# Performance work log

Measured on AMD Instinct MI355X. Metric: run time of the kernel, lower is better.

Reference implementation:

```python
import jax, jax.numpy as jnp
import numpy as np

B, T, C = 2, 4096, 512
H, DH = 8, 64            # num_heads, num_head_channels (per-head dim after reshape)
COND = 512
SCALE = (DH // H) ** -0.5  # faithful to original: (num_head_channels // num_heads)**-0.5


def setup_inputs() -> dict:
    key = jax.random.key(0)
    ks = jax.random.split(key, 6)
    x = jax.random.normal(ks[0], (B, T, C), dtype=jnp.float32)
    condition = jax.random.normal(ks[1], (B, T, COND), dtype=jnp.float32)
    W_qk = jax.random.normal(ks[2], (COND, 2 * H * DH), dtype=jnp.float32) * (COND ** -0.5)
    W_v = jax.random.normal(ks[3], (C, H * DH), dtype=jnp.float32) * (C ** -0.5)
    W_u = jax.random.normal(ks[4], (H * DH, C), dtype=jnp.float32) * ((H * DH) ** -0.5)
    b_u = jax.random.normal(ks[5], (C,), dtype=jnp.float32) * 0.01
    return {"x": x, "condition": condition, "W_qk": W_qk, "W_v": W_v, "W_u": W_u, "b_u": b_u}


def reference(x, condition, W_qk, W_v, W_u, b_u):
    b, t, _ = x.shape
    qk = condition @ W_qk                                  # [b, t, 2*H*DH]
    q, k = jnp.split(qk, 2, axis=-1)
    q = q.reshape(b, t, H, DH).transpose(0, 2, 1, 3)       # [b, H, t, DH]
    k = k.reshape(b, t, H, DH).transpose(0, 2, 1, 3)
    v = (x @ W_v).reshape(b, t, H, DH).transpose(0, 2, 1, 3)
    q = q * SCALE
    dots = jnp.einsum('bhid,bhjd->bhij', q, k)             # [b, H, t, t] (1 GB score matrix)
    attn = jax.nn.softmax(dots, axis=-1)
    out = jnp.einsum('bhij,bhjd->bhid', attn, v)           # [b, H, t, DH]
    out = out.transpose(0, 2, 1, 3).reshape(b, t, H * DH)
    return out @ W_u + b_u
```

## Files before the change

### kernel.cpp

```cpp
#include <hip/hip_runtime.h>

#define B_SZ 2
#define T_SZ 4096

typedef unsigned short u16;
typedef __attribute__((ext_vector_type(8))) short short8;
typedef __attribute__((ext_vector_type(4))) float f32x4;
typedef __attribute__((ext_vector_type(4))) unsigned short u16x4;

#define CEXP 0.51006973f

__device__ __forceinline__ u16 f2bf(float f) {
    unsigned int u;
    __builtin_memcpy(&u, &f, 4);
    u = (u + 0x7fffu + ((u >> 16) & 1u)) >> 16;
    return (u16)u;
}
__device__ __forceinline__ unsigned int rbits(float f) {
    unsigned int u;
    __builtin_memcpy(&u, &f, 4);
    return u + 0x8000u;
}
__device__ __forceinline__ f32x4 mfma16(short8 a, short8 b, f32x4 c) {
    return __builtin_amdgcn_mfma_f32_16x16x32_bf16(a, b, c, 0, 0, 0);
}

__global__ void k_prep(const float* __restrict__ Wqk, const float* __restrict__ Wv,
                       const float* __restrict__ Wu, u16* __restrict__ Wqk_t,
                       u16* __restrict__ Wv_t, u16* __restrict__ Wu_t) {
    int blk = blockIdx.x;
    if (blk < 2048) {
        int idx = blk * 256 + threadIdx.x;
        Wqk_t[(size_t)(idx & 1023) * 512 + (idx >> 10)] = f2bf(Wqk[idx]);
    } else if (blk < 3072) {
        int idx = (blk - 2048) * 256 + threadIdx.x;
        Wv_t[(size_t)(idx & 511) * 512 + (idx >> 9)] = f2bf(Wv[idx]);
    } else {
        int idx = (blk - 3072) * 256 + threadIdx.x;
        Wu_t[(size_t)(idx & 511) * 512 + (idx >> 9)] = f2bf(Wu[idx]);
    }
}

template <typename OutT, int MODE, bool AF32, bool BF32, int TM, int TN>
__global__ __launch_bounds__(256) void k_gemm4(const void* __restrict__ Ap, const void* __restrict__ Bp,
                                               const float* __restrict__ bias, OutT* __restrict__ C,
                                               OutT* __restrict__ C2) {
    const int K = 512;
    constexpr int MI = TM / 32, NJ = TN / 32;
    constexpr int NAF = TM / 32, NAB = TM / 64;
    constexpr int NBF = TN / 32, NBB = TN / 64;
    int m0 = blockIdx.x * TM, n0 = blockIdx.y * TN;
    int tid = threadIdx.x;
    int wave = tid >> 6, lane = tid & 63, l16 = lane & 15, q = lane >> 4;
    int mo = (wave & 1) * (TM / 2), no = (wave >> 1) * (TN / 2);

    __shared__ __align__(16) u16 As[TM * 72];
    __shared__ __align__(16) u16 Bs[TN * 72];

    f32x4 acc[MI][NJ];
#pragma unroll
    for (int i = 0; i < MI; ++i)
#pragma unroll
        for (int j = 0; j < NJ; ++j) acc[i][j] = (f32x4){0.f, 0.f, 0.f, 0.f};

    const float* Af = (const float*)Ap; const u16* Ab = (const u16*)Ap;
    const float* Bf = (const float*)Bp; const u16* Bb = (const u16*)Bp;

    const float* apf[NAF > 0 ? NAF : 1]; const u16* apb[NAB > 0 ? NAB : 1];
    const float* bpf[NBF > 0 ? NBF : 1]; const u16* bpb[NBB > 0 ? NBB : 1];
    float4 raf[NAF > 0 ? NAF : 1], rbf[NBF > 0 ? NBF : 1];
    short8 rab[NAB > 0 ? NAB : 1], rbb[NBB > 0 ? NBB : 1];

    if constexpr (AF32) {
#pragma unroll
        for (int jj = 0; jj < NAF; ++jj) {
            int id = tid + 256 * jj;
            apf[jj] = Af + (size_t)(m0 + (id >> 3)) * K + (id & 7) * 4;
            raf[jj] = *(const float4*)(apf[jj]);
        }
    } else {
#pragma unroll
        for (int jj = 0; jj < NAB; ++jj) {
            int id = tid + 256 * jj;
            apb[jj] = Ab + (size_t)(m0 + (id >> 2)) * K + (id & 3) * 8;
            rab[jj] = *(const short8*)(apb[jj]);
        }
    }
    if constexpr (BF32) {
#pragma unroll
        for (int jj = 0; jj < NBF; ++jj) {
            int id = tid + 256 * jj;
            bpf[jj] = Bf + (size_t)(n0 + (id >> 3)) * K + (id & 7) * 4;
            rbf[jj] = *(const float4*)(bpf[jj]);
        }
    } else {
#pragma unroll
        for (int jj = 0; jj < NBB; ++jj) {
            int id = tid + 256 * jj;
            bpb[jj] = Bb + (size_t)(n0 + (id >> 2)) * K + (id & 3) * 8;
            rbb[jj] = *(const short8*)(bpb[jj]);
        }
    }

#pragma unroll 1
    for (int k0 = 0; k0 < K; k0 += 32) {
        __syncthreads();
        if constexpr (AF32) {
#pragma unroll
            for (int jj = 0; jj < NAF; ++jj) {
                int id = tid + 256 * jj;
                u16x4 w = { f2bf(raf[jj].x), f2bf(raf[jj].y), f2bf(raf[jj].z), f2bf(raf[jj].w) };
                *(u16x4*)(&As[(id >> 3) * 72 + (id & 7) * 4]) = w;
            }
        } else {
#pragma unroll
            for (int jj = 0; jj < NAB; ++jj) {
                int id = tid + 256 * jj;
                *(short8*)(&As[(id >> 2) * 72 + (id & 3) * 8]) = rab[jj];
            }
        }
        if constexpr (BF32) {
#pragma unroll
            for (int jj = 0; jj < NBF; ++jj) {
                int id = tid + 256 * jj;
                u16x4 w = { f2bf(rbf[jj].x), f2bf(rbf[jj].y), f2bf(rbf[jj].z), f2bf(rbf[jj].w) };
                *(u16x4*)(&Bs[(id >> 3) * 72 + (id & 7) * 4]) = w;
            }
        } else {
#pragma unroll
            for (int jj = 0; jj < NBB; ++jj) {
                int id = tid + 256 * jj;
                *(short8*)(&Bs[(id >> 2) * 72 + (id & 3) * 8]) = rbb[jj];
            }
        }
        __syncthreads();

        int kadv = (k0 + 32 < K) ? 32 : 0;
        if constexpr (AF32) {
#pragma unroll
            for (int jj = 0; jj < NAF; ++jj) { apf[jj] += kadv; raf[jj] = *(const float4*)(apf[jj]); }
        } else {
#pragma unroll
            for (int jj = 0; jj < NAB; ++jj) { apb[jj] += kadv; rab[jj] = *(const short8*)(apb[jj]); }
        }
        if constexpr (BF32) {
#pragma unroll
            for (int jj = 0; jj < NBF; ++jj) { bpf[jj] += kadv; rbf[jj] = *(const float4*)(bpf[jj]); }
        } else {
#pragma unroll
            for (int jj = 0; jj < NBB; ++jj) { bpb[jj] += kadv; rbb[jj] = *(const short8*)(bpb[jj]); }
        }
        __builtin_amdgcn_sched_barrier(0);

        short8 af[MI], bf[NJ];
#pragma unroll
        for (int i = 0; i < MI; ++i) af[i] = *(const short8*)(&As[(mo + i * 16 + l16) * 72 + q * 8]);
#pragma unroll
        for (int j = 0; j < NJ; ++j) bf[j] = *(const short8*)(&Bs[(no + j * 16 + l16) * 72 + q * 8]);
#pragma unroll
        for (int i = 0; i < MI; ++i)
#pragma unroll
            for (int j = 0; j < NJ; ++j) acc[i][j] = mfma16(af[i], bf[j], acc[i][j]);
    }

#pragma unroll
    for (int i = 0; i < MI; ++i) {
        int mb = m0 + mo + i * 16 + q * 4;
#pragma unroll
        for (int j = 0; j < NJ; ++j) {
            int nc = n0 + no + j * 16 + l16;
            if constexpr (MODE == 0) {
                float4 bb = *(const float4*)(bias + mb);
                float4 w = { acc[i][j][0] + bb.x, acc[i][j][1] + bb.y,
                             acc[i][j][2] + bb.z, acc[i][j][3] + bb.w };
                *(float4*)(&C[(size_t)nc * 512 + mb]) = w;
            } else if constexpr (MODE == 1) {
                int b = nc >> 12, t = nc & 4095;
                int h = (mb & 511) >> 6, d = mb & 63;
                size_t addr = ((size_t)((b * 8 + h) * 4096 + t)) * 64 + d;
                if (mb < 512) {
                    u16x4 w = { f2bf(acc[i][j][0] * CEXP), f2bf(acc[i][j][1] * CEXP),
                                f2bf(acc[i][j][2] * CEXP), f2bf(acc[i][j][3] * CEXP) };
                    *(u16x4*)(&C[addr]) = w;
                } else {
                    u16x4 w = { f2bf(acc[i][j][0]), f2bf(acc[i][j][1]),
                                f2bf(acc[i][j][2]), f2bf(acc[i][j][3]) };
                    *(u16x4*)(&C2[addr]) = w;
                }
            } else {
                int b = mb >> 12, t = mb & 4095;
                int kt = t >> 6, k64 = t & 63;
                int h = nc >> 6, d = nc & 63;
                size_t addr = ((((size_t)(b * 8 + h) * 64 + kt) * 64 + d) << 6) + k64;
                u16x4 w = { f2bf(acc[i][j][0]), f2bf(acc[i][j][1]),
                            f2bf(acc[i][j][2]), f2bf(acc[i][j][3]) };
                *(u16x4*)(&C[addr]) = w;
            }
        }
    }
}

__global__ __launch_bounds__(256) void k_flash(const u16* __restrict__ Qh, const u16* __restrict__ Kh,
                                               const u16* __restrict__ Vb, u16* __restrict__ o) {
    int bid = blockIdx.x;
    int h = bid & 7, qt = (bid >> 3) & 63, b = bid >> 9;
    int tid = threadIdx.x;
    int wave = tid >> 6, lane = tid & 63, l16 = lane & 15, q = lane >> 4;

    __shared__ __align__(16) u16 Kt[64 * 80];
    __shared__ __align__(16) u16 Vt[64 * 72];

    int head = b * 8 + h;
    const u16* qp = Qh + ((size_t)head * 4096 + qt * 64 + wave * 16 + l16) * 64 + q * 8;
    short8 qf0 = *(const short8*)(qp);
    short8 qf1 = *(const short8*)(qp + 32);

    const u16* kb = Kh + (size_t)head * 4096 * 64;
    const u16* vb = Vb + (size_t)head * 4096 * 64;

    int r0 = tid >> 3, g0 = tid & 7;
    u16* kw0 = &Kt[r0 * 80 + g0 * 8];
    u16* kw1 = &Kt[(r0 + 32) * 80 + g0 * 8];
    u16* vw0 = &Vt[r0 * 72 + g0 * 8];
    u16* vw1 = &Vt[(r0 + 32) * 72 + g0 * 8];

    f32x4 oacc[4];
#pragma unroll
    for (int c = 0; c < 4; ++c) oacc[c] = (f32x4){0.f, 0.f, 0.f, 0.f};
    f32x4 lacc = (f32x4){0.f, 0.f, 0.f, 0.f};
    const short8 ones = { 0x3F80, 0x3F80, 0x3F80, 0x3F80, 0x3F80, 0x3F80, 0x3F80, 0x3F80 };
    int pi0 = (l16 >> 2) * 8 + (l16 & 3);

    size_t off0 = (size_t)qt * 4096;
    short8 rk0 = *(const short8*)(kb + off0 + tid * 8);
    short8 rk1 = *(const short8*)(kb + off0 + tid * 8 + 2048);
    short8 rv0 = *(const short8*)(vb + off0 + tid * 8);
    short8 rv1 = *(const short8*)(vb + off0 + tid * 8 + 2048);

#pragma unroll 1
    for (int it = 0; it < 64; ++it) {
        __syncthreads();
        *(short8*)kw0 = rk0;
        *(short8*)kw1 = rk1;
        *(short8*)vw0 = rv0;
        *(short8*)vw1 = rv1;
        __syncthreads();

        size_t offn = (size_t)((qt + it + 1) & 63) * 4096;
        rk0 = *(const short8*)(kb + offn + tid * 8);
        rk1 = *(const short8*)(kb + offn + tid * 8 + 2048);
        rv0 = *(const short8*)(vb + offn + tid * 8);
        rv1 = *(const short8*)(vb + offn + tid * 8 + 2048);
        __builtin_amdgcn_sched_barrier(0);

#pragma unroll
        for (int kk = 0; kk < 2; ++kk) {
            const u16* ka = &Kt[(kk * 32 + pi0) * 80 + q * 8];
            short8 A00 = *(const short8*)(ka);
            short8 A01 = *(const short8*)(ka + 32);
            short8 A10 = *(const short8*)(ka + 4 * 80);
            short8 A11 = *(const short8*)(ka + 4 * 80 + 32);
            f32x4 s0 = (f32x4){0.f, 0.f, 0.f, 0.f};
            f32x4 s1 = (f32x4){0.f, 0.f, 0.f, 0.f};
            s0 = mfma16(A00, qf0, s0); s0 = mfma16(A01, qf1, s0);
            s1 = mfma16(A10, qf0, s1); s1 = mfma16(A11, qf1, s1);

            uint4 pd;
            pd.x = __builtin_amdgcn_perm(rbits(__builtin_amdgcn_exp2f(s0[1])),
                                         rbits(__builtin_amdgcn_exp2f(s0[0])), 0x07060302u);
            pd.y = __builtin_amdgcn_perm(rbits(__builtin_amdgcn_exp2f(s0[3])),
                                         rbits(__builtin_amdgcn_exp2f(s0[2])), 0x07060302u);
            pd.z = __builtin_amdgcn_perm(rbits(__builtin_amdgcn_exp2f(s1[1])),
                                         rbits(__builtin_amdgcn_exp2f(s1[0])), 0x07060302u);
            pd.w = __builtin_amdgcn_perm(rbits(__builtin_amdgcn_exp2f(s1[3])),
                                         rbits(__builtin_amdgcn_exp2f(s1[2])), 0x07060302u);
            short8 pf;
            __builtin_memcpy(&pf, &pd, 16);

            lacc = mfma16(ones, pf, lacc);
#pragma unroll
            for (int c = 0; c < 4; ++c) {
                short8 vfc = *(const short8*)(&Vt[(c * 16 + l16) * 72 + kk * 32 + q * 8]);
                oacc[c] = mfma16(vfc, pf, oacc[c]);
            }
        }
    }

    float inv = 1.f / lacc[0];

    u16* ob = o + (size_t)(b * T_SZ + qt * 64 + wave * 16 + l16) * 512 + h * 64 + q * 4;
#pragma unroll
    for (int c = 0; c < 4; ++c) {
        u16x4 w = { f2bf(oacc[c][0] * inv), f2bf(oacc[c][1] * inv),
                    f2bf(oacc[c][2] * inv), f2bf(oacc[c][3] * inv) };
        *(u16x4*)(ob + c * 16) = w;
    }
}

extern "C" void kernel_launch(void* const* d_in, const int* in_sizes, int n_in,
                              void* d_out, int out_size, void* d_ws, size_t ws_size,
                              hipStream_t stream) {
    const float* x    = (const float*)d_in[0];
    const float* cond = (const float*)d_in[1];
    const float* Wqk  = (const float*)d_in[2];
    const float* Wv   = (const float*)d_in[3];
    const float* Wu   = (const float*)d_in[4];
    const float* bu   = (const float*)d_in[5];
    float* out = (float*)d_out;

    const size_t MT = (size_t)B_SZ * T_SZ;
    u16* qh_ws = (u16*)d_ws;
    u16* kh_ws = qh_ws + MT * 512;
    u16* vb_ws = kh_ws + MT * 512;
    u16* at_ws = vb_ws + MT * 512;
    u16* Wqk_t = at_ws + MT * 512;
    u16* Wv_t  = Wqk_t + (size_t)1024 * 512;
    u16* Wu_t  = Wv_t + (size_t)512 * 512;

    k_prep<<<4096, 256, 0, stream>>>(Wqk, Wv, Wu, Wqk_t, Wv_t, Wu_t);

    k_gemm4<u16, 1, false, true, 256, 64><<<dim3(4, 128), 256, 0, stream>>>(Wqk_t, cond, nullptr, qh_ws, kh_ws);
    k_gemm4<u16, 2, true, false, 64, 128><<<dim3(128, 4), 256, 0, stream>>>(x, Wv_t, nullptr, vb_ws, nullptr);
    k_flash<<<1024, 256, 0, stream>>>(qh_ws, kh_ws, vb_ws, at_ws);
    k_gemm4<float, 0, false, false, 128, 64><<<dim3(4, 128), 256, 0, stream>>>(Wu_t, at_ws, bu, out, nullptr);
}
```

Baseline: 243.2 us.

## Process two query tiles per flash block to reuse K/V shared-memory loads

Each flash-attention block now handles 128 query rows (two 64-row groups) instead of 64. Every K/V tile staged in LDS, and the V fragments read from it, then serve both groups. This halves global K/V traffic and the LDS staging/sync work per unit of compute. The grid shrinks from 1024 to 512 blocks, and per-thread accumulators double, which raises register pressure and may reduce occupancy and load balance on a 256-CU device.

```diff
diff --git a/kernel.cpp b/kernel.cpp
--- a/kernel.cpp
+++ b/kernel.cpp
@@ -203,7 +203,7 @@
 __global__ __launch_bounds__(256) void k_flash(const u16* __restrict__ Qh, const u16* __restrict__ Kh,
                                                const u16* __restrict__ Vb, u16* __restrict__ o) {
     int bid = blockIdx.x;
-    int h = bid & 7, qt = (bid >> 3) & 63, b = bid >> 9;
+    int h = bid & 7, qt = (bid >> 3) & 31, b = bid >> 8;
     int tid = threadIdx.x;
     int wave = tid >> 6, lane = tid & 63, l16 = lane & 15, q = lane >> 4;
 
@@ -211,9 +211,13 @@
     __shared__ __align__(16) u16 Vt[64 * 72];
 
     int head = b * 8 + h;
-    const u16* qp = Qh + ((size_t)head * 4096 + qt * 64 + wave * 16 + l16) * 64 + q * 8;
-    short8 qf0 = *(const short8*)(qp);
-    short8 qf1 = *(const short8*)(qp + 32);
+    short8 qf[2][2];
+#pragma unroll
+    for (int g = 0; g < 2; ++g) {
+        const u16* qp = Qh + ((size_t)head * 4096 + qt * 128 + g * 64 + wave * 16 + l16) * 64 + q * 8;
+        qf[g][0] = *(const short8*)(qp);
+        qf[g][1] = *(const short8*)(qp + 32);
+    }
 
     const u16* kb = Kh + (size_t)head * 4096 * 64;
     const u16* vb = Vb + (size_t)head * 4096 * 64;
@@ -224,14 +228,19 @@
     u16* vw0 = &Vt[r0 * 72 + g0 * 8];
     u16* vw1 = &Vt[(r0 + 32) * 72 + g0 * 8];
 
-    f32x4 oacc[4];
-#pragma unroll
-    for (int c = 0; c < 4; ++c) oacc[c] = (f32x4){0.f, 0.f, 0.f, 0.f};
-    f32x4 lacc = (f32x4){0.f, 0.f, 0.f, 0.f};
+    f32x4 oacc[2][4];
+#pragma unroll
+    for (int g = 0; g < 2; ++g)
+#pragma unroll
+        for (int c = 0; c < 4; ++c) oacc[g][c] = (f32x4){0.f, 0.f, 0.f, 0.f};
+    f32x4 lacc[2];
+    lacc[0] = (f32x4){0.f, 0.f, 0.f, 0.f};
+    lacc[1] = (f32x4){0.f, 0.f, 0.f, 0.f};
     const short8 ones = { 0x3F80, 0x3F80, 0x3F80, 0x3F80, 0x3F80, 0x3F80, 0x3F80, 0x3F80 };
     int pi0 = (l16 >> 2) * 8 + (l16 & 3);
 
-    size_t off0 = (size_t)qt * 4096;
+    int start = qt * 2;
+    size_t off0 = (size_t)((start) & 63) * 4096;
     short8 rk0 = *(const short8*)(kb + off0 + tid * 8);
     short8 rk1 = *(const short8*)(kb + off0 + tid * 8 + 2048);
     short8 rv0 = *(const short8*)(vb + off0 + tid * 8);
@@ -246,7 +255,7 @@
         *(short8*)vw1 = rv1;
         __syncthreads();
 
-        size_t offn = (size_t)((qt + it + 1) & 63) * 4096;
+        size_t offn = (size_t)((start + it + 1) & 63) * 4096;
         rk0 = *(const short8*)(kb + offn + tid * 8);
         rk1 = *(const short8*)(kb + offn + tid * 8 + 2048);
         rv0 = *(const short8*)(vb + offn + tid * 8);
@@ -260,40 +269,48 @@
             short8 A01 = *(const short8*)(ka + 32);
             short8 A10 = *(const short8*)(ka + 4 * 80);
             short8 A11 = *(const short8*)(ka + 4 * 80 + 32);
-            f32x4 s0 = (f32x4){0.f, 0.f, 0.f, 0.f};
-            f32x4 s1 = (f32x4){0.f, 0.f, 0.f, 0.f};
-            s0 = mfma16(A00, qf0, s0); s0 = mfma16(A01, qf1, s0);
-            s1 = mfma16(A10, qf0, s1); s1 = mfma16(A11, qf1, s1);
-
-            uint4 pd;
-            pd.x = __builtin_amdgcn_perm(rbits(__builtin_amdgcn_exp2f(s0[1])),
-                                         rbits(__builtin_amdgcn_exp2f(s0[0])), 0x07060302u);
-            pd.y = __builtin_amdgcn_perm(rbits(__builtin_amdgcn_exp2f(s0[3])),
-                                         rbits(__builtin_amdgcn_exp2f(s0[2])), 0x07060302u);
-            pd.z = __builtin_amdgcn_perm(rbits(__builtin_amdgcn_exp2f(s1[1])),
-                                         rbits(__builtin_amdgcn_exp2f(s1[0])), 0x07060302u);
-            pd.w = __builtin_amdgcn_perm(rbits(__builtin_amdgcn_exp2f(s1[3])),
-                                         rbits(__builtin_amdgcn_exp2f(s1[2])), 0x07060302u);
-            short8 pf;
-            __builtin_memcpy(&pf, &pd, 16);
-
-            lacc = mfma16(ones, pf, lacc);
-#pragma unroll
-            for (int c = 0; c < 4; ++c) {
-                short8 vfc = *(const short8*)(&Vt[(c * 16 + l16) * 72 + kk * 32 + q * 8]);
-                oacc[c] = mfma16(vfc, pf, oacc[c]);
-            }
-        }
-    }
-
-    float inv = 1.f / lacc[0];
-
-    u16* ob = o + (size_t)(b * T_SZ + qt * 64 + wave * 16 + l16) * 512 + h * 64 + q * 4;
-#pragma unroll
-    for (int c = 0; c < 4; ++c) {
-        u16x4 w = { f2bf(oacc[c][0] * inv), f2bf(oacc[c][1] * inv),
-                    f2bf(oacc[c][2] * inv), f2bf(oacc[c][3] * inv) };
-        *(u16x4*)(ob + c * 16) = w;
+            short8 vfc[4];
+#pragma unroll
+            for (int c = 0; c < 4; ++c)
+                vfc[c] = *(const short8*)(&Vt[(c * 16 + l16) * 72 + kk * 32 + q * 8]);
+
+#pragma unroll
+            for (int g = 0; g < 2; ++g) {
+                f32x4 s0 = (f32x4){0.f, 0.f, 0.f, 0.f};
+                f32x4 s1 = (f32x4){0.f, 0.f, 0.f, 0.f};
+                s0 = mfma16(A00, qf[g][0], s0); s0 = mfma16(A01, qf[g][1], s0);
+                s1 = mfma16(A10, qf[g][0], s1); s1 = mfma16(A11, qf[g][1], s1);
+
+                uint4 pd;
+                pd.x = __builtin_amdgcn_perm(rbits(__builtin_amdgcn_exp2f(s0[1])),
+                                             rbits(__builtin_amdgcn_exp2f(s0[0])), 0x07060302u);
+                pd.y = __builtin_amdgcn_perm(rbits(__builtin_amdgcn_exp2f(s0[3])),
+                                             rbits(__builtin_amdgcn_exp2f(s0[2])), 0x07060302u);
+                pd.z = __builtin_amdgcn_perm(rbits(__builtin_amdgcn_exp2f(s1[1])),
+                                             rbits(__builtin_amdgcn_exp2f(s1[0])), 0x07060302u);
+                pd.w = __builtin_amdgcn_perm(rbits(__builtin_amdgcn_exp2f(s1[3])),
+                                             rbits(__builtin_amdgcn_exp2f(s1[2])), 0x07060302u);
+                short8 pf;
+                __builtin_memcpy(&pf, &pd, 16);
+
+                lacc[g] = mfma16(ones, pf, lacc[g]);
+#pragma unroll
+                for (int c = 0; c < 4; ++c)
+                    oacc[g][c] = mfma16(vfc[c], pf, oacc[g][c]);
+            }
+        }
+    }
+
+#pragma unroll
+    for (int g = 0; g < 2; ++g) {
+        float inv = 1.f / lacc[g][0];
+        u16* ob = o + (size_t)(b * T_SZ + qt * 128 + g * 64 + wave * 16 + l16) * 512 + h * 64 + q * 4;
+#pragma unroll
+        for (int c = 0; c < 4; ++c) {
+            u16x4 w = { f2bf(oacc[g][c][0] * inv), f2bf(oacc[g][c][1] * inv),
+                        f2bf(oacc[g][c][2] * inv), f2bf(oacc[g][c][3] * inv) };
+            *(u16x4*)(ob + c * 16) = w;
+        }
     }
 }
 
@@ -321,6 +338,6 @@
 
     k_gemm4<u16, 1, false, true, 256, 64><<<dim3(4, 128), 256, 0, stream>>>(Wqk_t, cond, nullptr, qh_ws, kh_ws);
     k_gemm4<u16, 2, true, false, 64, 128><<<dim3(128, 4), 256, 0, stream>>>(x, Wv_t, nullptr, vb_ws, nullptr);
-    k_flash<<<1024, 256, 0, stream>>>(qh_ws, kh_ws, vb_ws, at_ws);
+    k_flash<<<512, 256, 0, stream>>>(qh_ws, kh_ws, vb_ws, at_ws);
     k_gemm4<float, 0, false, false, 128, 64><<<dim3(4, 128), 256, 0, stream>>>(Wu_t, at_ws, bu, out, nullptr);
 }
```

Result: faster. 235.2 us (-3.3%).
